# Kernel tuning notes

Measured on AMD Instinct MI355X. Metric: run time of the kernel, lower is better.

Reference implementation:

```python
import jax, jax.numpy as jnp
import numpy as np

N_NODES = 100000
N_EDGES = 1600000
N_GRAPHS = 256
HIDDEN = 256
ADD_FEATURES = 7
BN_EPS = 1e-5


def setup_inputs() -> dict:
    key = jax.random.key(0)
    ks = jax.random.split(key, 12)
    x = jax.random.normal(ks[0], (N_NODES, 1), dtype=jnp.float32)
    edge_index = jax.random.randint(ks[1], (2, N_EDGES), 0, N_NODES, dtype=jnp.int32)
    batch = jnp.sort(jax.random.randint(ks[2], (N_NODES,), 0, N_GRAPHS, dtype=jnp.int32))
    y_feat = jax.random.normal(ks[3], (N_GRAPHS, ADD_FEATURES), dtype=jnp.float32)
    # learned parameters
    W_conv = jax.random.normal(ks[4], (1, HIDDEN), dtype=jnp.float32) * 0.5
    b_conv = jnp.zeros((HIDDEN,), dtype=jnp.float32)
    gamma = jnp.ones((HIDDEN,), dtype=jnp.float32)
    beta = jnp.zeros((HIDDEN,), dtype=jnp.float32)
    W1 = jax.random.normal(ks[5], (HIDDEN + ADD_FEATURES, 128), dtype=jnp.float32) * (1.0 / np.sqrt(HIDDEN + ADD_FEATURES))
    b1 = jnp.zeros((128,), dtype=jnp.float32)
    W2 = jax.random.normal(ks[6], (128, 2), dtype=jnp.float32) * (1.0 / np.sqrt(128))
    b2 = jnp.zeros((2,), dtype=jnp.float32)
    return {"x": x, "edge_index": edge_index, "batch": batch, "y_feat": y_feat,
            "W_conv": W_conv, "b_conv": b_conv, "gamma": gamma, "beta": beta,
            "W1": W1, "b1": b1, "W2": W2, "b2": b2}


def _gcn_conv(x, W, b, edge_index, n_nodes):
    # PyG GCNConv: add self-loops, symmetric normalization D^-1/2 (A+I) D^-1/2 (x W) + b
    loop = jnp.arange(n_nodes, dtype=edge_index.dtype)
    src = jnp.concatenate([edge_index[0], loop])
    dst = jnp.concatenate([edge_index[1], loop])
    deg = jax.ops.segment_sum(jnp.ones_like(dst, dtype=x.dtype), dst, num_segments=n_nodes)
    dinv = jnp.where(deg > 0, jax.lax.rsqrt(jnp.maximum(deg, 1e-12)), 0.0)
    norm = dinv[src] * dinv[dst]                      # [E+N]
    xw = x @ W                                        # [N, H]
    msg = xw[src] * norm[:, None]                     # gather [E+N, H]
    return jax.ops.segment_sum(msg, dst, num_segments=n_nodes) + b


def reference(x, edge_index, batch, y_feat, W_conv, b_conv, gamma, beta, W1, b1, W2, b2):
    n_nodes = x.shape[0]
    h = _gcn_conv(x, W_conv, b_conv, edge_index, n_nodes)      # [N, 256]
    h = jax.nn.gelu(h, approximate=False)
    # BatchNorm over nodes (training-mode batch stats, biased variance, eps=1e-5)
    mean = jnp.mean(h, axis=0)
    var = jnp.mean(jnp.square(h - mean), axis=0)
    h = (h - mean) * jax.lax.rsqrt(var + BN_EPS) * gamma + beta
    # global mean pool by graph id
    sums = jax.ops.segment_sum(h, batch, num_segments=N_GRAPHS)           # [G, 256]
    counts = jax.ops.segment_sum(jnp.ones((n_nodes,), h.dtype), batch, num_segments=N_GRAPHS)
    pooled = sums / jnp.maximum(counts, 1.0)[:, None]
    g = jnp.concatenate([pooled, y_feat], axis=1)               # [G, 263]
    g = jax.nn.gelu(g @ W1 + b1, approximate=False)             # [G, 128]
    out = jax.nn.sigmoid(g @ W2 + b2)                           # [G, 2]
    return out
```

## Files before the change

kernel.cpp:

```cpp
#include <hip/hip_runtime.h>
#include <hip/hip_bf16.h>

#define HID 256
#define ADDF 7
#define MLP1 128
#define BN_EPS 1e-5f
#define NREP 8

#define NB 512
#define BW 196
#define BCAP 4096
#define PC 4096
#define PT 256
#define NW 4

__device__ __forceinline__ float gelu_fast(float z) {
    float z2 = z * z;
    float y2 = z * fmaf(0.07135481627f, z2, 1.59576912161f);
    float u  = __expf(fminf(y2, 80.0f));
    return z * u * __builtin_amdgcn_rcpf(u + 1.0f);
}

__global__ void k_init(float* zp, int nz, int* binCur,
                       const int* __restrict__ batch, int* __restrict__ cnt, int N, int G) {
    const int nzBlocks = (nz + 255) / 256;
    if ((int)blockIdx.x < nzBlocks) {
        int i = blockIdx.x * 256 + threadIdx.x;
        if (i < nz) zp[i] = 0.0f;
    } else {
        const int t = threadIdx.x;
        for (int b = t; b < NB; b += 256) binCur[b] = b * BCAP;
        if (t < G) {
            int lo = 0, hi = N;
            while (lo < hi) { int mid = (lo + hi) >> 1; if (batch[mid] < t) lo = mid + 1; else hi = mid; }
            int start = lo;
            lo = 0; hi = N;
            while (lo < hi) { int mid = (lo + hi) >> 1; if (batch[mid] < t + 1) lo = mid + 1; else hi = mid; }
            cnt[t] = lo - start;
        }
    }
}

__global__ __launch_bounds__(PT) void k_place(
        const int* __restrict__ src, const int* __restrict__ dst,
        int* __restrict__ binCur, int* __restrict__ recs, int E) {
    __shared__ int hist[NW][NB];
    const int t = threadIdx.x;
    const int w = t >> 6;
    for (int k = t; k < NW * NB; k += PT) (&hist[0][0])[k] = 0;
    __syncthreads();

    const int s0 = blockIdx.x * PC;
    const int e0 = min(s0 + PC, E);
    const bool vec = ((E & 3) == 0);
    const int n4 = vec ? ((e0 - s0) >> 2) : 0;
    const int4* dst4 = (const int4*)(dst + s0);
    const int4* src4 = (const int4*)(src + s0);

    for (int q = t; q < n4; q += PT) {
        int4 d = dst4[q];
        atomicAdd(&hist[w][d.x / BW], 1);
        atomicAdd(&hist[w][d.y / BW], 1);
        atomicAdd(&hist[w][d.z / BW], 1);
        atomicAdd(&hist[w][d.w / BW], 1);
    }
    for (int i = s0 + (n4 << 2) + t; i < e0; i += PT)
        atomicAdd(&hist[w][dst[i] / BW], 1);
    __syncthreads();

    for (int bb = t; bb < NB; bb += PT) {
        int b = (bb + ((int)blockIdx.x << 4)) & (NB - 1);
        int c0 = hist[0][b], c1 = hist[1][b], c2 = hist[2][b], c3 = hist[3][b];
        int tot = c0 + c1 + c2 + c3;
        int base = tot ? atomicAdd(&binCur[b], tot) : 0;
        hist[0][b] = base;
        hist[1][b] = base + c0;
        hist[2][b] = base + c0 + c1;
        hist[3][b] = base + c0 + c1 + c2;
    }
    __syncthreads();

    for (int q = t; q < n4; q += PT) {
        int4 d = dst4[q];
        int4 s = src4[q];
        int bin, pos;
        bin = d.x / BW; pos = atomicAdd(&hist[w][bin], 1); recs[pos] = ((d.x - bin * BW) << 17) | s.x;
        bin = d.y / BW; pos = atomicAdd(&hist[w][bin], 1); recs[pos] = ((d.y - bin * BW) << 17) | s.y;
        bin = d.z / BW; pos = atomicAdd(&hist[w][bin], 1); recs[pos] = ((d.z - bin * BW) << 17) | s.z;
        bin = d.w / BW; pos = atomicAdd(&hist[w][bin], 1); recs[pos] = ((d.w - bin * BW) << 17) | s.w;
    }
    for (int i = s0 + (n4 << 2) + t; i < e0; i += PT) {
        int d = dst[i];
        int bin = d / BW;
        int pos = atomicAdd(&hist[w][bin], 1);
        recs[pos] = ((d - bin * BW) << 17) | src[i];
    }
}

__global__ __launch_bounds__(256) void k_degv(
        const int* __restrict__ recs, const int* __restrict__ binCur,
        const float* __restrict__ x, float* __restrict__ dinv, float* __restrict__ v, int N) {
    __shared__ int degL[BW];
    const int b = blockIdx.x;
    const int t = threadIdx.x;
    if (t < BW) degL[t] = 0;
    __syncthreads();

    const int start = b * BCAP;
    const int end   = binCur[b];
    const int n4 = (end - start) >> 2;
    const int4* r4 = (const int4*)(recs + start);
    for (int q = t; q < n4; q += 256) {
        int4 r = r4[q];
        atomicAdd(&degL[r.x >> 17], 1);
        atomicAdd(&degL[r.y >> 17], 1);
        atomicAdd(&degL[r.z >> 17], 1);
        atomicAdd(&degL[r.w >> 17], 1);
    }
    for (int i = start + (n4 << 2) + t; i < end; i += 256)
        atomicAdd(&degL[recs[i] >> 17], 1);
    __syncthreads();

    int node = b * BW + t;
    if (t < BW && node < N) {
        float di = rsqrtf((float)degL[t] + 1.0f);
        dinv[node] = di;
        v[node]    = di * x[node];
    }
}

__global__ __launch_bounds__(HID) void k_agg_gelu(
        const int* __restrict__ recs, const int* __restrict__ binCur,
        const float* __restrict__ v, const float* __restrict__ dinv,
        const int* __restrict__ batch,
        const float* __restrict__ Wc, const float* __restrict__ bc,
        float* __restrict__ Sgj, float* __restrict__ Trep, float* __restrict__ T2rep, int N) {
    __shared__ float aggL[BW];
    __shared__ float sh_s[BW];
    __shared__ int   sh_b[BW];
    const int b = blockIdx.x;
    const int t = threadIdx.x;
    if (t < BW) aggL[t] = 0.0f;
    __syncthreads();

    const int start = b * BCAP;
    const int end   = binCur[b];
    const int n4 = (end - start) >> 2;
    const int4* r4 = (const int4*)(recs + start);
    for (int q = t; q < n4; q += 256) {
        int4 r = r4[q];
        atomicAdd(&aggL[r.x >> 17], v[r.x & 0x1FFFF]);
        atomicAdd(&aggL[r.y >> 17], v[r.y & 0x1FFFF]);
        atomicAdd(&aggL[r.z >> 17], v[r.z & 0x1FFFF]);
        atomicAdd(&aggL[r.w >> 17], v[r.w & 0x1FFFF]);
    }
    for (int i = start + (n4 << 2) + t; i < end; i += 256) {
        int rec = recs[i];
        atomicAdd(&aggL[rec >> 17], v[rec & 0x1FFFF]);
    }
    __syncthreads();

    const int node0 = b * BW;
    const int count = min(BW, N - node0);
    if (count <= 0) return;

    if (t < count) {
        int node = node0 + t;
        sh_s[t] = dinv[node] * (aggL[t] + v[node]);
        sh_b[t] = batch[node];
    }
    __syncthreads();

    const float wa = Wc[t];
    const float wb = bc[t];
    float tsum = 0.f, t2sum = 0.f, gsum = 0.f;
    int gid = sh_b[0];
    int n = 0;
    for (; n + 2 <= count; n += 2) {
        float h0 = gelu_fast(fmaf(sh_s[n],     wa, wb));
        float h1 = gelu_fast(fmaf(sh_s[n + 1], wa, wb));
        int b0 = sh_b[n], b1v = sh_b[n + 1];
        tsum += h0 + h1; t2sum += fmaf(h0, h0, h1 * h1);
        if (b0 != gid)  { atomicAdd(&Sgj[gid * HID + t], gsum); gsum = 0.f; gid = b0; }
        gsum += h0;
        if (b1v != gid) { atomicAdd(&Sgj[gid * HID + t], gsum); gsum = 0.f; gid = b1v; }
        gsum += h1;
    }
    if (n < count) {
        float h0 = gelu_fast(fmaf(sh_s[n], wa, wb));
        tsum += h0; t2sum += h0 * h0;
        int b0 = sh_b[n];
        if (b0 != gid) { atomicAdd(&Sgj[gid * HID + t], gsum); gsum = 0.f; gid = b0; }
        gsum += h0;
    }
    atomicAdd(&Sgj[gid * HID + t], gsum);
    const int r = b & (NREP - 1);
    atomicAdd(&Trep [r * HID + t], tsum);
    atomicAdd(&T2rep[r * HID + t], t2sum);
}

__global__ __launch_bounds__(HID) void k_pool_mlp(
        const float* __restrict__ Sgj, const float* __restrict__ Trep, const float* __restrict__ T2rep,
        const int* __restrict__ cnt, const float* __restrict__ gamma, const float* __restrict__ beta,
        const float* __restrict__ yfeat,
        const float* __restrict__ W1, const float* __restrict__ b1,
        const float* __restrict__ W2, const float* __restrict__ b2,
        float* __restrict__ out, int N) {
    __shared__ float gv[HID + ADDF];
    __shared__ float hid[MLP1];
    const int g = blockIdx.x;
    const int t = threadIdx.x;

    float Ts = 0.f, T2s = 0.f;
    #pragma unroll
    for (int r = 0; r < NREP; ++r) { Ts += Trep[r * HID + t]; T2s += T2rep[r * HID + t]; }
    float invN = 1.0f / (float)N;
    float mean = Ts * invN;
    float var  = fmaf(-mean, mean, T2s * invN);
    float rinv = rsqrtf(var + BN_EPS);
    float c = (float)max(cnt[g], 1);
    gv[t] = (Sgj[g * HID + t] / c - mean) * rinv * gamma[t] + beta[t];
    if (t < ADDF) gv[HID + t] = yfeat[g * ADDF + t];
    __syncthreads();

    if (t < MLP1) {
        float acc = b1[t];
        #pragma unroll 8
        for (int k = 0; k < HID + ADDF; ++k)
            acc = fmaf(gv[k], W1[k * MLP1 + t], acc);
        hid[t] = gelu_fast(acc);
    }
    __syncthreads();

    if (t < 2) {
        float o = b2[t];
        for (int k = 0; k < MLP1; ++k)
            o = fmaf(hid[k], W2[k * 2 + t], o);
        out[g * 2 + t] = 1.0f / (1.0f + expf(-o));
    }
}

__global__ void k_zero(float* p, int n) {
    for (int i = blockIdx.x * blockDim.x + threadIdx.x; i < n; i += gridDim.x * blockDim.x)
        p[i] = 0.0f;
}
__global__ void k_deg_fb(const int* __restrict__ dst, float* __restrict__ deg, int E) {
    int i = blockIdx.x * blockDim.x + threadIdx.x;
    if (i < E) atomicAdd(&deg[dst[i]], 1.0f);
}
__global__ void k_dinv_fb(float* __restrict__ deg, const float* __restrict__ x,
                          float* __restrict__ v, int N) {
    int i = blockIdx.x * blockDim.x + threadIdx.x;
    if (i < N) { float di = rsqrtf(deg[i] + 1.0f); deg[i] = di; v[i] = di * x[i]; }
}
__global__ void k_scatter_fb(const int* __restrict__ src, const int* __restrict__ dst,
                             const float* __restrict__ v, float* __restrict__ agg, int E) {
    int i = blockIdx.x * blockDim.x + threadIdx.x;
    if (i < E) atomicAdd(&agg[dst[i]], v[src[i]]);
}
#define CHUNK_FB 64
__global__ __launch_bounds__(HID) void k_gelu_fb(
        const float* __restrict__ v, const float* __restrict__ dinv,
        const float* __restrict__ agg, const int* __restrict__ batch,
        const float* __restrict__ Wc, const float* __restrict__ bc,
        float* __restrict__ Sgj, float* __restrict__ Trep, float* __restrict__ T2rep, int N) {
    __shared__ float sh_s[CHUNK_FB];
    __shared__ int   sh_b[CHUNK_FB];
    const int j = threadIdx.x;
    const int base = blockIdx.x * CHUNK_FB;
    const int count = min(CHUNK_FB, N - base);
    if (j < count) {
        int i = base + j;
        sh_s[j] = dinv[i] * (agg[i] + v[i]);
        sh_b[j] = batch[i];
    }
    __syncthreads();
    const float a = Wc[j];
    const float b = bc[j];
    float tsum = 0.f, t2sum = 0.f, gsum = 0.f;
    int gid = sh_b[0];
    for (int n = 0; n < count; ++n) {
        float h = gelu_fast(fmaf(sh_s[n], a, b));
        tsum += h; t2sum += h * h;
        int bg = sh_b[n];
        if (bg != gid) { atomicAdd(&Sgj[gid * HID + j], gsum); gsum = 0.f; gid = bg; }
        gsum += h;
    }
    atomicAdd(&Sgj[gid * HID + j], gsum);
    const int r = blockIdx.x & (NREP - 1);
    atomicAdd(&Trep [r * HID + j], tsum);
    atomicAdd(&T2rep[r * HID + j], t2sum);
}

extern "C" void kernel_launch(void* const* d_in, const int* in_sizes, int n_in,
                              void* d_out, int out_size, void* d_ws, size_t ws_size,
                              hipStream_t stream) {
    const float* x     = (const float*)d_in[0];
    const int*   edge  = (const int*)  d_in[1];
    const int*   batch = (const int*)  d_in[2];
    const float* yfeat = (const float*)d_in[3];
    const float* Wc    = (const float*)d_in[4];
    const float* bc    = (const float*)d_in[5];
    const float* gamma = (const float*)d_in[6];
    const float* beta  = (const float*)d_in[7];
    const float* W1    = (const float*)d_in[8];
    const float* b1    = (const float*)d_in[9];
    const float* W2    = (const float*)d_in[10];
    const float* b2    = (const float*)d_in[11];
    float* out = (float*)d_out;

    const int N = in_sizes[0];
    const int E = in_sizes[1] / 2;
    const int G = in_sizes[3] / ADDF;

    const int* srcIdx = edge;
    const int* dstIdx = edge + E;

    float* ws     = (float*)d_ws;
    float* Sgj    = ws;
    float* Trep   = Sgj + (size_t)G * HID;
    float* T2rep  = Trep + NREP * HID;
    int*   cnt    = (int*)(T2rep + NREP * HID);
    int*   binCur = cnt + G;
    float* dinv   = (float*)(binCur + NB);
    float* v      = dinv + (size_t)NB * BW;
    int*   recs   = (int*)(v + (size_t)NB * BW);

    const size_t headF  = (size_t)G * HID + 2 * NREP * HID + G + NB;
    const size_t needT1 = (headF + 2 * (size_t)NB * BW + (size_t)NB * BCAP) * 4;
    const int zeroCount = G * HID + 2 * NREP * HID;
    const int initBlocks = (zeroCount + 255) / 256 + 1;

    if (ws_size >= needT1 && N <= NB * BW) {
        k_init<<<initBlocks, 256, 0, stream>>>(Sgj, zeroCount, binCur, batch, cnt, N, G);
        k_place<<<(E + PC - 1) / PC, PT, 0, stream>>>(srcIdx, dstIdx, binCur, recs, E);
        k_degv<<<NB, 256, 0, stream>>>(recs, binCur, x, dinv, v, N);
        k_agg_gelu<<<NB, HID, 0, stream>>>(recs, binCur, v, dinv, batch, Wc, bc, Sgj, Trep, T2rep, N);
    } else {
        float* degA = (float*)(binCur + NB);
        float* vA   = degA + N;
        float* aggA = vA + N;
        k_init<<<initBlocks, 256, 0, stream>>>(Sgj, zeroCount, binCur, batch, cnt, N, G);
        k_zero<<<512, 256, 0, stream>>>(degA, N);
        k_zero<<<512, 256, 0, stream>>>(aggA, N);
        k_deg_fb<<<(E + 255) / 256, 256, 0, stream>>>(dstIdx, degA, E);
        k_dinv_fb<<<(N + 255) / 256, 256, 0, stream>>>(degA, x, vA, N);
        k_scatter_fb<<<(E + 255) / 256, 256, 0, stream>>>(srcIdx, dstIdx, vA, aggA, E);
        k_gelu_fb<<<(N + CHUNK_FB - 1) / CHUNK_FB, HID, 0, stream>>>(vA, degA, aggA, batch, Wc, bc, Sgj, Trep, T2rep, N);
    }

    k_pool_mlp<<<G, HID, 0, stream>>>(Sgj, Trep, T2rep, cnt, gamma, beta, yfeat, W1, b1, W2, b2, out, N);
}
```

Baseline: 86.40 us.

## Fuse all stages into one cooperative persistent kernel with grid syncs

Replaces the five separate launches (init, place, degree, aggregate+gelu, pool+MLP) with a single cooperative kernel of 512 blocks that separates the stages with grid-wide syncs. Edge placement now uses one chunk per block instead of 4096-edge chunks, so each block handles about 3125 edges. The aim is to remove launch overhead and inter-kernel gaps. In exchange it adds grid.sync costs, relies on all 512 blocks being co-resident, and gives less parallelism to the placement and MLP stages.

```diff
diff --git a/kernel.cpp b/kernel.cpp
--- a/kernel.cpp
+++ b/kernel.cpp
@@ -1,5 +1,8 @@
 #include <hip/hip_runtime.h>
+#include <hip/hip_cooperative_groups.h>
 #include <hip/hip_bf16.h>
+
+namespace cg = cooperative_groups;
 
 #define HID 256
 #define ADDF 7
@@ -10,8 +13,6 @@
 #define NB 512
 #define BW 196
 #define BCAP 4096
-#define PC 4096
-#define PT 256
 #define NW 4
 
 __device__ __forceinline__ float gelu_fast(float z) {
@@ -21,15 +22,238 @@
     return z * u * __builtin_amdgcn_rcpf(u + 1.0f);
 }
 
-__global__ void k_init(float* zp, int nz, int* binCur,
-                       const int* __restrict__ batch, int* __restrict__ cnt, int N, int G) {
+__global__ __launch_bounds__(256, 2) void k_mega(
+        const float* __restrict__ x, const int* __restrict__ src, const int* __restrict__ dst,
+        const int* __restrict__ batch, const float* __restrict__ yfeat,
+        const float* __restrict__ Wc, const float* __restrict__ bc,
+        const float* __restrict__ gamma, const float* __restrict__ beta,
+        const float* __restrict__ W1, const float* __restrict__ b1,
+        const float* __restrict__ W2, const float* __restrict__ b2,
+        float* __restrict__ out,
+        float* __restrict__ Sgj, float* __restrict__ Trep, float* __restrict__ T2rep,
+        int* __restrict__ cnt, int* __restrict__ binCur,
+        float* __restrict__ dinv, float* __restrict__ v, int* __restrict__ recs,
+        int N, int E, int G) {
+    cg::grid_group grid = cg::this_grid();
+    __shared__ int smbuf[NW * NB];
+    const int t = threadIdx.x;
+    const int b = blockIdx.x;
+    const int nblk = (int)gridDim.x;
+
+    {
+        const int zc = G * HID + 2 * NREP * HID;
+        const int gt = b * 256 + t;
+        const int tot = nblk * 256;
+        for (int i = gt; i < zc; i += tot) Sgj[i] = 0.0f;
+        if (gt < NB) binCur[gt] = gt * BCAP;
+        const int g = gt - NB;
+        if (g >= 0 && g < G) {
+            int lo = 0, hi = N;
+            while (lo < hi) { int mid = (lo + hi) >> 1; if (batch[mid] < g) lo = mid + 1; else hi = mid; }
+            int start = lo;
+            lo = 0; hi = N;
+            while (lo < hi) { int mid = (lo + hi) >> 1; if (batch[mid] < g + 1) lo = mid + 1; else hi = mid; }
+            cnt[g] = lo - start;
+        }
+    }
+    grid.sync();
+
+    {
+        const int pcm = (((E + nblk - 1) / nblk) + 3) & ~3;
+        const int s0 = b * pcm;
+        const int e0 = min(s0 + pcm, E);
+        int (*hist)[NB] = (int(*)[NB])smbuf;
+        const int w = t >> 6;
+        for (int k = t; k < NW * NB; k += 256) smbuf[k] = 0;
+        __syncthreads();
+
+        bool al = false; int n4 = 0;
+        if (s0 < e0) {
+            al = (((((uintptr_t)(dst + s0)) | ((uintptr_t)(src + s0))) & 15) == 0);
+            n4 = al ? ((e0 - s0) >> 2) : 0;
+            const int4* dst4 = (const int4*)(dst + s0);
+            for (int q = t; q < n4; q += 256) {
+                int4 d = dst4[q];
+                atomicAdd(&hist[w][d.x / BW], 1);
+                atomicAdd(&hist[w][d.y / BW], 1);
+                atomicAdd(&hist[w][d.z / BW], 1);
+                atomicAdd(&hist[w][d.w / BW], 1);
+            }
+            for (int i = s0 + (n4 << 2) + t; i < e0; i += 256)
+                atomicAdd(&hist[w][dst[i] / BW], 1);
+        }
+        __syncthreads();
+
+        for (int bb = t; bb < NB; bb += 256) {
+            int bi = (bb + (b << 4)) & (NB - 1);
+            int c0 = hist[0][bi], c1 = hist[1][bi], c2 = hist[2][bi], c3 = hist[3][bi];
+            int tot4 = c0 + c1 + c2 + c3;
+            int base = tot4 ? atomicAdd(&binCur[bi], tot4) : 0;
+            hist[0][bi] = base;
+            hist[1][bi] = base + c0;
+            hist[2][bi] = base + c0 + c1;
+            hist[3][bi] = base + c0 + c1 + c2;
+        }
+        __syncthreads();
+
+        if (s0 < e0) {
+            const int4* dst4 = (const int4*)(dst + s0);
+            const int4* src4 = (const int4*)(src + s0);
+            for (int q = t; q < n4; q += 256) {
+                int4 d = dst4[q];
+                int4 s = src4[q];
+                int bin, pos;
+                bin = d.x / BW; pos = atomicAdd(&hist[w][bin], 1); recs[pos] = ((d.x - bin * BW) << 17) | s.x;
+                bin = d.y / BW; pos = atomicAdd(&hist[w][bin], 1); recs[pos] = ((d.y - bin * BW) << 17) | s.y;
+                bin = d.z / BW; pos = atomicAdd(&hist[w][bin], 1); recs[pos] = ((d.z - bin * BW) << 17) | s.z;
+                bin = d.w / BW; pos = atomicAdd(&hist[w][bin], 1); recs[pos] = ((d.w - bin * BW) << 17) | s.w;
+            }
+            for (int i = s0 + (n4 << 2) + t; i < e0; i += 256) {
+                int d = dst[i];
+                int bin = d / BW;
+                int pos = atomicAdd(&hist[w][bin], 1);
+                recs[pos] = ((d - bin * BW) << 17) | src[i];
+            }
+        }
+    }
+    grid.sync();
+
+    {
+        int* degL = smbuf;
+        if (t < BW) degL[t] = 0;
+        __syncthreads();
+
+        const int start = b * BCAP;
+        const int end   = binCur[b];
+        const int n4 = (end - start) >> 2;
+        const int4* r4 = (const int4*)(recs + start);
+        for (int q = t; q < n4; q += 256) {
+            int4 r = r4[q];
+            atomicAdd(&degL[r.x >> 17], 1);
+            atomicAdd(&degL[r.y >> 17], 1);
+            atomicAdd(&degL[r.z >> 17], 1);
+            atomicAdd(&degL[r.w >> 17], 1);
+        }
+        for (int i = start + (n4 << 2) + t; i < end; i += 256)
+            atomicAdd(&degL[recs[i] >> 17], 1);
+        __syncthreads();
+
+        int node = b * BW + t;
+        if (t < BW && node < N) {
+            float di = rsqrtf((float)degL[t] + 1.0f);
+            dinv[node] = di;
+            v[node]    = di * x[node];
+        }
+    }
+    grid.sync();
+
+    {
+        float* aggL = (float*)smbuf;
+        float* sh_s = aggL + BW;
+        int*   sh_b = (int*)(sh_s + BW);
+        if (t < BW) aggL[t] = 0.0f;
+        __syncthreads();
+
+        const int start = b * BCAP;
+        const int end   = binCur[b];
+        const int n4 = (end - start) >> 2;
+        const int4* r4 = (const int4*)(recs + start);
+        for (int q = t; q < n4; q += 256) {
+            int4 r = r4[q];
+            atomicAdd(&aggL[r.x >> 17], v[r.x & 0x1FFFF]);
+            atomicAdd(&aggL[r.y >> 17], v[r.y & 0x1FFFF]);
+            atomicAdd(&aggL[r.z >> 17], v[r.z & 0x1FFFF]);
+            atomicAdd(&aggL[r.w >> 17], v[r.w & 0x1FFFF]);
+        }
+        for (int i = start + (n4 << 2) + t; i < end; i += 256) {
+            int rec = recs[i];
+            atomicAdd(&aggL[rec >> 17], v[rec & 0x1FFFF]);
+        }
+        __syncthreads();
+
+        const int node0 = b * BW;
+        const int count = min(BW, N - node0);
+        if (count > 0) {
+            if (t < count) {
+                int node = node0 + t;
+                sh_s[t] = dinv[node] * (aggL[t] + v[node]);
+                sh_b[t] = batch[node];
+            }
+            __syncthreads();
+
+            const float wa = Wc[t];
+            const float wb = bc[t];
+            float tsum = 0.f, t2sum = 0.f, gsum = 0.f;
+            int gid = sh_b[0];
+            int n = 0;
+            for (; n + 2 <= count; n += 2) {
+                float h0 = gelu_fast(fmaf(sh_s[n],     wa, wb));
+                float h1 = gelu_fast(fmaf(sh_s[n + 1], wa, wb));
+                int b0 = sh_b[n], b1v = sh_b[n + 1];
+                tsum += h0 + h1; t2sum += fmaf(h0, h0, h1 * h1);
+                if (b0 != gid)  { atomicAdd(&Sgj[gid * HID + t], gsum); gsum = 0.f; gid = b0; }
+                gsum += h0;
+                if (b1v != gid) { atomicAdd(&Sgj[gid * HID + t], gsum); gsum = 0.f; gid = b1v; }
+                gsum += h1;
+            }
+            if (n < count) {
+                float h0 = gelu_fast(fmaf(sh_s[n], wa, wb));
+                tsum += h0; t2sum += h0 * h0;
+                int b0 = sh_b[n];
+                if (b0 != gid) { atomicAdd(&Sgj[gid * HID + t], gsum); gsum = 0.f; gid = b0; }
+                gsum += h0;
+            }
+            atomicAdd(&Sgj[gid * HID + t], gsum);
+            const int r = b & (NREP - 1);
+            atomicAdd(&Trep [r * HID + t], tsum);
+            atomicAdd(&T2rep[r * HID + t], t2sum);
+        }
+    }
+    grid.sync();
+
+    for (int g = b; g < G; g += nblk) {
+        float* gv  = (float*)smbuf;
+        float* hid = gv + HID + ADDF;
+
+        float Ts = 0.f, T2s = 0.f;
+        #pragma unroll
+        for (int r = 0; r < NREP; ++r) { Ts += Trep[r * HID + t]; T2s += T2rep[r * HID + t]; }
+        float invN = 1.0f / (float)N;
+        float mean = Ts * invN;
+        float var  = fmaf(-mean, mean, T2s * invN);
+        float rinv = rsqrtf(var + BN_EPS);
+        float c = (float)max(cnt[g], 1);
+        gv[t] = (Sgj[g * HID + t] / c - mean) * rinv * gamma[t] + beta[t];
+        if (t < ADDF) gv[HID + t] = yfeat[g * ADDF + t];
+        __syncthreads();
+
+        if (t < MLP1) {
+            float acc = b1[t];
+            #pragma unroll 8
+            for (int k = 0; k < HID + ADDF; ++k)
+                acc = fmaf(gv[k], W1[k * MLP1 + t], acc);
+            hid[t] = gelu_fast(acc);
+        }
+        __syncthreads();
+
+        if (t < 2) {
+            float o = b2[t];
+            for (int k = 0; k < MLP1; ++k)
+                o = fmaf(hid[k], W2[k * 2 + t], o);
+            out[g * 2 + t] = 1.0f / (1.0f + expf(-o));
+        }
+        __syncthreads();
+    }
+}
+
+__global__ void k_init_fb(float* zp, int nz, const int* __restrict__ batch,
+                          int* __restrict__ cnt, int N, int G) {
     const int nzBlocks = (nz + 255) / 256;
     if ((int)blockIdx.x < nzBlocks) {
         int i = blockIdx.x * 256 + threadIdx.x;
         if (i < nz) zp[i] = 0.0f;
     } else {
         const int t = threadIdx.x;
-        for (int b = t; b < NB; b += 256) binCur[b] = b * BCAP;
         if (t < G) {
             int lo = 0, hi = N;
             while (lo < hi) { int mid = (lo + hi) >> 1; if (batch[mid] < t) lo = mid + 1; else hi = mid; }
@@ -40,206 +264,6 @@
         }
     }
 }
-
-__global__ __launch_bounds__(PT) void k_place(
-        const int* __restrict__ src, const int* __restrict__ dst,
-        int* __restrict__ binCur, int* __restrict__ recs, int E) {
-    __shared__ int hist[NW][NB];
-    const int t = threadIdx.x;
-    const int w = t >> 6;
-    for (int k = t; k < NW * NB; k += PT) (&hist[0][0])[k] = 0;
-    __syncthreads();
-
-    const int s0 = blockIdx.x * PC;
-    const int e0 = min(s0 + PC, E);
-    const bool vec = ((E & 3) == 0);
-    const int n4 = vec ? ((e0 - s0) >> 2) : 0;
-    const int4* dst4 = (const int4*)(dst + s0);
-    const int4* src4 = (const int4*)(src + s0);
-
-    for (int q = t; q < n4; q += PT) {
-        int4 d = dst4[q];
-        atomicAdd(&hist[w][d.x / BW], 1);
-        atomicAdd(&hist[w][d.y / BW], 1);
-        atomicAdd(&hist[w][d.z / BW], 1);
-        atomicAdd(&hist[w][d.w / BW], 1);
-    }
-    for (int i = s0 + (n4 << 2) + t; i < e0; i += PT)
-        atomicAdd(&hist[w][dst[i] / BW], 1);
-    __syncthreads();
-
-    for (int bb = t; bb < NB; bb += PT) {
-        int b = (bb + ((int)blockIdx.x << 4)) & (NB - 1);
-        int c0 = hist[0][b], c1 = hist[1][b], c2 = hist[2][b], c3 = hist[3][b];
-        int tot = c0 + c1 + c2 + c3;
-        int base = tot ? atomicAdd(&binCur[b], tot) : 0;
-        hist[0][b] = base;
-        hist[1][b] = base + c0;
-        hist[2][b] = base + c0 + c1;
-        hist[3][b] = base + c0 + c1 + c2;
-    }
-    __syncthreads();
-
-    for (int q = t; q < n4; q += PT) {
-        int4 d = dst4[q];
-        int4 s = src4[q];
-        int bin, pos;
-        bin = d.x / BW; pos = atomicAdd(&hist[w][bin], 1); recs[pos] = ((d.x - bin * BW) << 17) | s.x;
-        bin = d.y / BW; pos = atomicAdd(&hist[w][bin], 1); recs[pos] = ((d.y - bin * BW) << 17) | s.y;
-        bin = d.z / BW; pos = atomicAdd(&hist[w][bin], 1); recs[pos] = ((d.z - bin * BW) << 17) | s.z;
-        bin = d.w / BW; pos = atomicAdd(&hist[w][bin], 1); recs[pos] = ((d.w - bin * BW) << 17) | s.w;
-    }
-    for (int i = s0 + (n4 << 2) + t; i < e0; i += PT) {
-        int d = dst[i];
-        int bin = d / BW;
-        int pos = atomicAdd(&hist[w][bin], 1);
-        recs[pos] = ((d - bin * BW) << 17) | src[i];
-    }
-}
-
-__global__ __launch_bounds__(256) void k_degv(
-        const int* __restrict__ recs, const int* __restrict__ binCur,
-        const float* __restrict__ x, float* __restrict__ dinv, float* __restrict__ v, int N) {
-    __shared__ int degL[BW];
-    const int b = blockIdx.x;
-    const int t = threadIdx.x;
-    if (t < BW) degL[t] = 0;
-    __syncthreads();
-
-    const int start = b * BCAP;
-    const int end   = binCur[b];
-    const int n4 = (end - start) >> 2;
-    const int4* r4 = (const int4*)(recs + start);
-    for (int q = t; q < n4; q += 256) {
-        int4 r = r4[q];
-        atomicAdd(&degL[r.x >> 17], 1);
-        atomicAdd(&degL[r.y >> 17], 1);
-        atomicAdd(&degL[r.z >> 17], 1);
-        atomicAdd(&degL[r.w >> 17], 1);
-    }
-    for (int i = start + (n4 << 2) + t; i < end; i += 256)
-        atomicAdd(&degL[recs[i] >> 17], 1);
-    __syncthreads();
-
-    int node = b * BW + t;
-    if (t < BW && node < N) {
-        float di = rsqrtf((float)degL[t] + 1.0f);
-        dinv[node] = di;
-        v[node]    = di * x[node];
-    }
-}
-
-__global__ __launch_bounds__(HID) void k_agg_gelu(
-        const int* __restrict__ recs, const int* __restrict__ binCur,
-        const float* __restrict__ v, const float* __restrict__ dinv,
-        const int* __restrict__ batch,
-        const float* __restrict__ Wc, const float* __restrict__ bc,
-        float* __restrict__ Sgj, float* __restrict__ Trep, float* __restrict__ T2rep, int N) {
-    __shared__ float aggL[BW];
-    __shared__ float sh_s[BW];
-    __shared__ int   sh_b[BW];
-    const int b = blockIdx.x;
-    const int t = threadIdx.x;
-    if (t < BW) aggL[t] = 0.0f;
-    __syncthreads();
-
-    const int start = b * BCAP;
-    const int end   = binCur[b];
-    const int n4 = (end - start) >> 2;
-    const int4* r4 = (const int4*)(recs + start);
-    for (int q = t; q < n4; q += 256) {
-        int4 r = r4[q];
-        atomicAdd(&aggL[r.x >> 17], v[r.x & 0x1FFFF]);
-        atomicAdd(&aggL[r.y >> 17], v[r.y & 0x1FFFF]);
-        atomicAdd(&aggL[r.z >> 17], v[r.z & 0x1FFFF]);
-        atomicAdd(&aggL[r.w >> 17], v[r.w & 0x1FFFF]);
-    }
-    for (int i = start + (n4 << 2) + t; i < end; i += 256) {
-        int rec = recs[i];
-        atomicAdd(&aggL[rec >> 17], v[rec & 0x1FFFF]);
-    }
-    __syncthreads();
-
-    const int node0 = b * BW;
-    const int count = min(BW, N - node0);
-    if (count <= 0) return;
-
-    if (t < count) {
-        int node = node0 + t;
-        sh_s[t] = dinv[node] * (aggL[t] + v[node]);
-        sh_b[t] = batch[node];
-    }
-    __syncthreads();
-
-    const float wa = Wc[t];
-    const float wb = bc[t];
-    float tsum = 0.f, t2sum = 0.f, gsum = 0.f;
-    int gid = sh_b[0];
-    int n = 0;
-    for (; n + 2 <= count; n += 2) {
-        float h0 = gelu_fast(fmaf(sh_s[n],     wa, wb));
-        float h1 = gelu_fast(fmaf(sh_s[n + 1], wa, wb));
-        int b0 = sh_b[n], b1v = sh_b[n + 1];
-        tsum += h0 + h1; t2sum += fmaf(h0, h0, h1 * h1);
-        if (b0 != gid)  { atomicAdd(&Sgj[gid * HID + t], gsum); gsum = 0.f; gid = b0; }
-        gsum += h0;
-        if (b1v != gid) { atomicAdd(&Sgj[gid * HID + t], gsum); gsum = 0.f; gid = b1v; }
-        gsum += h1;
-    }
-    if (n < count) {
-        float h0 = gelu_fast(fmaf(sh_s[n], wa, wb));
-        tsum += h0; t2sum += h0 * h0;
-        int b0 = sh_b[n];
-        if (b0 != gid) { atomicAdd(&Sgj[gid * HID + t], gsum); gsum = 0.f; gid = b0; }
-        gsum += h0;
-    }
-    atomicAdd(&Sgj[gid * HID + t], gsum);
-    const int r = b & (NREP - 1);
-    atomicAdd(&Trep [r * HID + t], tsum);
-    atomicAdd(&T2rep[r * HID + t], t2sum);
-}
-
-__global__ __launch_bounds__(HID) void k_pool_mlp(
-        const float* __restrict__ Sgj, const float* __restrict__ Trep, const float* __restrict__ T2rep,
-        const int* __restrict__ cnt, const float* __restrict__ gamma, const float* __restrict__ beta,
-        const float* __restrict__ yfeat,
-        const float* __restrict__ W1, const float* __restrict__ b1,
-        const float* __restrict__ W2, const float* __restrict__ b2,
-        float* __restrict__ out, int N) {
-    __shared__ float gv[HID + ADDF];
-    __shared__ float hid[MLP1];
-    const int g = blockIdx.x;
-    const int t = threadIdx.x;
-
-    float Ts = 0.f, T2s = 0.f;
-    #pragma unroll
-    for (int r = 0; r < NREP; ++r) { Ts += Trep[r * HID + t]; T2s += T2rep[r * HID + t]; }
-    float invN = 1.0f / (float)N;
-    float mean = Ts * invN;
-    float var  = fmaf(-mean, mean, T2s * invN);
-    float rinv = rsqrtf(var + BN_EPS);
-    float c = (float)max(cnt[g], 1);
-    gv[t] = (Sgj[g * HID + t] / c - mean) * rinv * gamma[t] + beta[t];
-    if (t < ADDF) gv[HID + t] = yfeat[g * ADDF + t];
-    __syncthreads();
-
-    if (t < MLP1) {
-        float acc = b1[t];
-        #pragma unroll 8
-        for (int k = 0; k < HID + ADDF; ++k)
-            acc = fmaf(gv[k], W1[k * MLP1 + t], acc);
-        hid[t] = gelu_fast(acc);
-    }
-    __syncthreads();
-
-    if (t < 2) {
-        float o = b2[t];
-        for (int k = 0; k < MLP1; ++k)
-            o = fmaf(hid[k], W2[k * 2 + t], o);
-        out[g * 2 + t] = 1.0f / (1.0f + expf(-o));
-    }
-}
-
 __global__ void k_zero(float* p, int n) {
     for (int i = blockIdx.x * blockDim.x + threadIdx.x; i < n; i += gridDim.x * blockDim.x)
         p[i] = 0.0f;
@@ -290,6 +314,43 @@
     const int r = blockIdx.x & (NREP - 1);
     atomicAdd(&Trep [r * HID + j], tsum);
     atomicAdd(&T2rep[r * HID + j], t2sum);
+}
+__global__ __launch_bounds__(HID) void k_pool_mlp_fb(
+        const float* __restrict__ Sgj, const float* __restrict__ Trep, const float* __restrict__ T2rep,
+        const int* __restrict__ cnt, const float* __restrict__ gamma, const float* __restrict__ beta,
+        const float* __restrict__ yfeat,
+        const float* __restrict__ W1, const float* __restrict__ b1,
+        const float* __restrict__ W2, const float* __restrict__ b2,
+        float* __restrict__ out, int N) {
+    __shared__ float gv[HID + ADDF];
+    __shared__ float hid[MLP1];
+    const int g = blockIdx.x;
+    const int t = threadIdx.x;
+    float Ts = 0.f, T2s = 0.f;
+    #pragma unroll
+    for (int r = 0; r < NREP; ++r) { Ts += Trep[r * HID + t]; T2s += T2rep[r * HID + t]; }
+    float invN = 1.0f / (float)N;
+    float mean = Ts * invN;
+    float var  = fmaf(-mean, mean, T2s * invN);
+    float rinv = rsqrtf(var + BN_EPS);
+    float c = (float)max(cnt[g], 1);
+    gv[t] = (Sgj[g * HID + t] / c - mean) * rinv * gamma[t] + beta[t];
+    if (t < ADDF) gv[HID + t] = yfeat[g * ADDF + t];
+    __syncthreads();
+    if (t < MLP1) {
+        float acc = b1[t];
+        #pragma unroll 8
+        for (int k = 0; k < HID + ADDF; ++k)
+            acc = fmaf(gv[k], W1[k * MLP1 + t], acc);
+        hid[t] = gelu_fast(acc);
+    }
+    __syncthreads();
+    if (t < 2) {
+        float o = b2[t];
+        for (int k = 0; k < MLP1; ++k)
+            o = fmaf(hid[k], W2[k * 2 + t], o);
+        out[g * 2 + t] = 1.0f / (1.0f + expf(-o));
+    }
 }
 
 extern "C" void kernel_launch(void* const* d_in, const int* in_sizes, int n_in,
@@ -309,9 +370,9 @@
     const float* b2    = (const float*)d_in[11];
     float* out = (float*)d_out;
 
-    const int N = in_sizes[0];
-    const int E = in_sizes[1] / 2;
-    const int G = in_sizes[3] / ADDF;
+    int N = in_sizes[0];
+    int E = in_sizes[1] / 2;
+    int G = in_sizes[3] / ADDF;
 
     const int* srcIdx = edge;
     const int* dstIdx = edge + E;
@@ -329,25 +390,28 @@
     const size_t headF  = (size_t)G * HID + 2 * NREP * HID + G + NB;
     const size_t needT1 = (headF + 2 * (size_t)NB * BW + (size_t)NB * BCAP) * 4;
     const int zeroCount = G * HID + 2 * NREP * HID;
-    const int initBlocks = (zeroCount + 255) / 256 + 1;
-
-    if (ws_size >= needT1 && N <= NB * BW) {
-        k_init<<<initBlocks, 256, 0, stream>>>(Sgj, zeroCount, binCur, batch, cnt, N, G);
-        k_place<<<(E + PC - 1) / PC, PT, 0, stream>>>(srcIdx, dstIdx, binCur, recs, E);
-        k_degv<<<NB, 256, 0, stream>>>(recs, binCur, x, dinv, v, N);
-        k_agg_gelu<<<NB, HID, 0, stream>>>(recs, binCur, v, dinv, batch, Wc, bc, Sgj, Trep, T2rep, N);
+
+    if (ws_size >= needT1 && N <= NB * BW && G <= 131072 - NB) {
+        void* args[] = {
+            (void*)&x, (void*)&srcIdx, (void*)&dstIdx, (void*)&batch, (void*)&yfeat,
+            (void*)&Wc, (void*)&bc, (void*)&gamma, (void*)&beta,
+            (void*)&W1, (void*)&b1, (void*)&W2, (void*)&b2, (void*)&out,
+            (void*)&Sgj, (void*)&Trep, (void*)&T2rep, (void*)&cnt, (void*)&binCur,
+            (void*)&dinv, (void*)&v, (void*)&recs, (void*)&N, (void*)&E, (void*)&G
+        };
+        hipLaunchCooperativeKernel((void*)k_mega, dim3(NB), dim3(256), args, 0, stream);
     } else {
         float* degA = (float*)(binCur + NB);
         float* vA   = degA + N;
         float* aggA = vA + N;
-        k_init<<<initBlocks, 256, 0, stream>>>(Sgj, zeroCount, binCur, batch, cnt, N, G);
+        const int initBlocks = (zeroCount + 255) / 256 + 1;
+        k_init_fb<<<initBlocks, 256, 0, stream>>>(Sgj, zeroCount, batch, cnt, N, G);
         k_zero<<<512, 256, 0, stream>>>(degA, N);
         k_zero<<<512, 256, 0, stream>>>(aggA, N);
         k_deg_fb<<<(E + 255) / 256, 256, 0, stream>>>(dstIdx, degA, E);
         k_dinv_fb<<<(N + 255) / 256, 256, 0, stream>>>(degA, x, vA, N);
         k_scatter_fb<<<(E + 255) / 256, 256, 0, stream>>>(srcIdx, dstIdx, vA, aggA, E);
         k_gelu_fb<<<(N + CHUNK_FB - 1) / CHUNK_FB, HID, 0, stream>>>(vA, degA, aggA, batch, Wc, bc, Sgj, Trep, T2rep, N);
-    }
-
-    k_pool_mlp<<<G, HID, 0, stream>>>(Sgj, Trep, T2rep, cnt, gamma, beta, yfeat, W1, b1, W2, b2, out, N);
-}
+        k_pool_mlp_fb<<<G, HID, 0, stream>>>(Sgj, Trep, T2rep, cnt, gamma, beta, yfeat, W1, b1, W2, b2, out, N);
+    }
+}
```

Result: slower. 305.2 us (+253.2%).

## Replace atomic bin placement with histogram, scan and deterministic store passes

Applied to the files above, without the earlier changes.

Splits the single-pass edge binning kernel into three kernels. A per-chunk histogram pass writes counts to global memory, a per-bin scan turns them into chunk offsets, and a store pass scatters the packed records. This removes the global atomicAdd on bin cursors and folds zeroing and graph counts into these kernels, though it reads the edge array twice and adds a launch. The degree and aggregation kernels move to 512 threads, with the GELU loop split across two halves of the node range, to raise parallelism per bin.

```diff
diff --git a/kernel.cpp b/kernel.cpp
--- a/kernel.cpp
+++ b/kernel.cpp
@@ -10,8 +10,7 @@
 #define NB 512
 #define BW 196
 #define BCAP 4096
-#define PC 4096
-#define PT 256
+#define PC 2048
 #define NW 4
 
 __device__ __forceinline__ float gelu_fast(float z) {
@@ -21,83 +20,118 @@
     return z * u * __builtin_amdgcn_rcpf(u + 1.0f);
 }
 
-__global__ void k_init(float* zp, int nz, int* binCur,
-                       const int* __restrict__ batch, int* __restrict__ cnt, int N, int G) {
-    const int nzBlocks = (nz + 255) / 256;
-    if ((int)blockIdx.x < nzBlocks) {
-        int i = blockIdx.x * 256 + threadIdx.x;
-        if (i < nz) zp[i] = 0.0f;
-    } else {
-        const int t = threadIdx.x;
-        for (int b = t; b < NB; b += 256) binCur[b] = b * BCAP;
-        if (t < G) {
-            int lo = 0, hi = N;
-            while (lo < hi) { int mid = (lo + hi) >> 1; if (batch[mid] < t) lo = mid + 1; else hi = mid; }
-            int start = lo;
-            lo = 0; hi = N;
-            while (lo < hi) { int mid = (lo + hi) >> 1; if (batch[mid] < t + 1) lo = mid + 1; else hi = mid; }
-            cnt[t] = lo - start;
+__global__ __launch_bounds__(256) void k_hist(
+        const int* __restrict__ dst, int* __restrict__ hist,
+        float* __restrict__ zbase, int zcount, int E, int nchunk, int cpx) {
+    __shared__ int h[NW][NB];
+    const int t = threadIdx.x;
+    const int bid = blockIdx.x;
+
+    int gt = bid * 256 + t;
+    if (gt < zcount) zbase[gt] = 0.0f;
+
+    const int m = (bid & 7) * cpx + (bid >> 3);
+    for (int k = t; k < NW * NB; k += 256) (&h[0][0])[k] = 0;
+    __syncthreads();
+
+    if (m < nchunk) {
+        const int s0 = m * PC;
+        const int e0 = min(s0 + PC, E);
+        const int w = t >> 6;
+        const bool al = ((((uintptr_t)(dst + s0)) & 15) == 0);
+        const int n4 = al ? ((e0 - s0) >> 2) : 0;
+        const int4* dst4 = (const int4*)(dst + s0);
+        for (int q = t; q < n4; q += 256) {
+            int4 d = dst4[q];
+            atomicAdd(&h[w][d.x / BW], 1);
+            atomicAdd(&h[w][d.y / BW], 1);
+            atomicAdd(&h[w][d.z / BW], 1);
+            atomicAdd(&h[w][d.w / BW], 1);
         }
-    }
-}
-
-__global__ __launch_bounds__(PT) void k_place(
+        for (int i = s0 + (n4 << 2) + t; i < e0; i += 256)
+            atomicAdd(&h[w][dst[i] / BW], 1);
+        __syncthreads();
+        for (int b = t; b < NB; b += 256)
+            hist[(size_t)m * NB + b] = h[0][b] + h[1][b] + h[2][b] + h[3][b];
+    }
+}
+
+__global__ __launch_bounds__(64) void k_scan(
+        int* __restrict__ hist, int* __restrict__ binCur,
+        const int* __restrict__ batch, int* __restrict__ cnt,
+        int nchunk, int N, int G) {
+    const int bin = blockIdx.x;
+    const int lane = threadIdx.x;
+    __shared__ int bounds[2];
+
+    if (bin < G && lane < 2) {
+        int target = bin + lane;
+        int lo = 0, hi = N;
+        while (lo < hi) { int mid = (lo + hi) >> 1; if (batch[mid] < target) lo = mid + 1; else hi = mid; }
+        bounds[lane] = lo;
+    }
+
+    const int per = (nchunk + 63) / 64;
+    const int m0 = lane * per;
+    const int m1 = min(m0 + per, nchunk);
+    int sum = 0;
+    for (int m = m0; m < m1; ++m) sum += hist[(size_t)m * NB + bin];
+
+    int incl = sum;
+    #pragma unroll
+    for (int d = 1; d < 64; d <<= 1) {
+        int o = __shfl_up(incl, d);
+        if (lane >= d) incl += o;
+    }
+    const int total = __shfl(incl, 63);
+    int run = bin * BCAP + (incl - sum);
+    for (int m = m0; m < m1; ++m) {
+        int c = hist[(size_t)m * NB + bin];
+        hist[(size_t)m * NB + bin] = run;
+        run += c;
+    }
+    if (lane == 63) binCur[bin] = bin * BCAP + total;
+
+    __syncthreads();
+    if (bin < G && lane == 0) cnt[bin] = bounds[1] - bounds[0];
+}
+
+__global__ __launch_bounds__(256) void k_store(
         const int* __restrict__ src, const int* __restrict__ dst,
-        int* __restrict__ binCur, int* __restrict__ recs, int E) {
-    __shared__ int hist[NW][NB];
+        const int* __restrict__ hist, int* __restrict__ recs,
+        int E, int nchunk, int cpx) {
+    __shared__ int cur[NB];
     const int t = threadIdx.x;
-    const int w = t >> 6;
-    for (int k = t; k < NW * NB; k += PT) (&hist[0][0])[k] = 0;
-    __syncthreads();
-
-    const int s0 = blockIdx.x * PC;
+    const int m = ((int)blockIdx.x & 7) * cpx + ((int)blockIdx.x >> 3);
+    if (m >= nchunk) return;
+
+    for (int b = t; b < NB; b += 256) cur[b] = hist[(size_t)m * NB + b];
+    __syncthreads();
+
+    const int s0 = m * PC;
     const int e0 = min(s0 + PC, E);
-    const bool vec = ((E & 3) == 0);
-    const int n4 = vec ? ((e0 - s0) >> 2) : 0;
+    const bool al = (((((uintptr_t)(dst + s0)) | ((uintptr_t)(src + s0))) & 15) == 0);
+    const int n4 = al ? ((e0 - s0) >> 2) : 0;
     const int4* dst4 = (const int4*)(dst + s0);
     const int4* src4 = (const int4*)(src + s0);
-
-    for (int q = t; q < n4; q += PT) {
-        int4 d = dst4[q];
-        atomicAdd(&hist[w][d.x / BW], 1);
-        atomicAdd(&hist[w][d.y / BW], 1);
-        atomicAdd(&hist[w][d.z / BW], 1);
-        atomicAdd(&hist[w][d.w / BW], 1);
-    }
-    for (int i = s0 + (n4 << 2) + t; i < e0; i += PT)
-        atomicAdd(&hist[w][dst[i] / BW], 1);
-    __syncthreads();
-
-    for (int bb = t; bb < NB; bb += PT) {
-        int b = (bb + ((int)blockIdx.x << 4)) & (NB - 1);
-        int c0 = hist[0][b], c1 = hist[1][b], c2 = hist[2][b], c3 = hist[3][b];
-        int tot = c0 + c1 + c2 + c3;
-        int base = tot ? atomicAdd(&binCur[b], tot) : 0;
-        hist[0][b] = base;
-        hist[1][b] = base + c0;
-        hist[2][b] = base + c0 + c1;
-        hist[3][b] = base + c0 + c1 + c2;
-    }
-    __syncthreads();
-
-    for (int q = t; q < n4; q += PT) {
+    for (int q = t; q < n4; q += 256) {
         int4 d = dst4[q];
         int4 s = src4[q];
         int bin, pos;
-        bin = d.x / BW; pos = atomicAdd(&hist[w][bin], 1); recs[pos] = ((d.x - bin * BW) << 17) | s.x;
-        bin = d.y / BW; pos = atomicAdd(&hist[w][bin], 1); recs[pos] = ((d.y - bin * BW) << 17) | s.y;
-        bin = d.z / BW; pos = atomicAdd(&hist[w][bin], 1); recs[pos] = ((d.z - bin * BW) << 17) | s.z;
-        bin = d.w / BW; pos = atomicAdd(&hist[w][bin], 1); recs[pos] = ((d.w - bin * BW) << 17) | s.w;
-    }
-    for (int i = s0 + (n4 << 2) + t; i < e0; i += PT) {
+        bin = d.x / BW; pos = atomicAdd(&cur[bin], 1); recs[pos] = ((d.x - bin * BW) << 17) | s.x;
+        bin = d.y / BW; pos = atomicAdd(&cur[bin], 1); recs[pos] = ((d.y - bin * BW) << 17) | s.y;
+        bin = d.z / BW; pos = atomicAdd(&cur[bin], 1); recs[pos] = ((d.z - bin * BW) << 17) | s.z;
+        bin = d.w / BW; pos = atomicAdd(&cur[bin], 1); recs[pos] = ((d.w - bin * BW) << 17) | s.w;
+    }
+    for (int i = s0 + (n4 << 2) + t; i < e0; i += 256) {
         int d = dst[i];
         int bin = d / BW;
-        int pos = atomicAdd(&hist[w][bin], 1);
+        int pos = atomicAdd(&cur[bin], 1);
         recs[pos] = ((d - bin * BW) << 17) | src[i];
     }
 }
 
-__global__ __launch_bounds__(256) void k_degv(
+__global__ __launch_bounds__(512) void k_degv(
         const int* __restrict__ recs, const int* __restrict__ binCur,
         const float* __restrict__ x, float* __restrict__ dinv, float* __restrict__ v, int N) {
     __shared__ int degL[BW];
@@ -110,14 +144,14 @@
     const int end   = binCur[b];
     const int n4 = (end - start) >> 2;
     const int4* r4 = (const int4*)(recs + start);
-    for (int q = t; q < n4; q += 256) {
+    for (int q = t; q < n4; q += 512) {
         int4 r = r4[q];
         atomicAdd(&degL[r.x >> 17], 1);
         atomicAdd(&degL[r.y >> 17], 1);
         atomicAdd(&degL[r.z >> 17], 1);
         atomicAdd(&degL[r.w >> 17], 1);
     }
-    for (int i = start + (n4 << 2) + t; i < end; i += 256)
+    for (int i = start + (n4 << 2) + t; i < end; i += 512)
         atomicAdd(&degL[recs[i] >> 17], 1);
     __syncthreads();
 
@@ -129,7 +163,7 @@
     }
 }
 
-__global__ __launch_bounds__(HID) void k_agg_gelu(
+__global__ __launch_bounds__(512) void k_agg_gelu(
         const int* __restrict__ recs, const int* __restrict__ binCur,
         const float* __restrict__ v, const float* __restrict__ dinv,
         const int* __restrict__ batch,
@@ -147,14 +181,14 @@
     const int end   = binCur[b];
     const int n4 = (end - start) >> 2;
     const int4* r4 = (const int4*)(recs + start);
-    for (int q = t; q < n4; q += 256) {
+    for (int q = t; q < n4; q += 512) {
         int4 r = r4[q];
         atomicAdd(&aggL[r.x >> 17], v[r.x & 0x1FFFF]);
         atomicAdd(&aggL[r.y >> 17], v[r.y & 0x1FFFF]);
         atomicAdd(&aggL[r.z >> 17], v[r.z & 0x1FFFF]);
         atomicAdd(&aggL[r.w >> 17], v[r.w & 0x1FFFF]);
     }
-    for (int i = start + (n4 << 2) + t; i < end; i += 256) {
+    for (int i = start + (n4 << 2) + t; i < end; i += 512) {
         int rec = recs[i];
         atomicAdd(&aggL[rec >> 17], v[rec & 0x1FFFF]);
     }
@@ -171,32 +205,37 @@
     }
     __syncthreads();
 
-    const float wa = Wc[t];
-    const float wb = bc[t];
-    float tsum = 0.f, t2sum = 0.f, gsum = 0.f;
-    int gid = sh_b[0];
-    int n = 0;
-    for (; n + 2 <= count; n += 2) {
-        float h0 = gelu_fast(fmaf(sh_s[n],     wa, wb));
-        float h1 = gelu_fast(fmaf(sh_s[n + 1], wa, wb));
-        int b0 = sh_b[n], b1v = sh_b[n + 1];
-        tsum += h0 + h1; t2sum += fmaf(h0, h0, h1 * h1);
-        if (b0 != gid)  { atomicAdd(&Sgj[gid * HID + t], gsum); gsum = 0.f; gid = b0; }
-        gsum += h0;
-        if (b1v != gid) { atomicAdd(&Sgj[gid * HID + t], gsum); gsum = 0.f; gid = b1v; }
-        gsum += h1;
-    }
-    if (n < count) {
-        float h0 = gelu_fast(fmaf(sh_s[n], wa, wb));
-        tsum += h0; t2sum += h0 * h0;
-        int b0 = sh_b[n];
-        if (b0 != gid) { atomicAdd(&Sgj[gid * HID + t], gsum); gsum = 0.f; gid = b0; }
-        gsum += h0;
-    }
-    atomicAdd(&Sgj[gid * HID + t], gsum);
-    const int r = b & (NREP - 1);
-    atomicAdd(&Trep [r * HID + t], tsum);
-    atomicAdd(&T2rep[r * HID + t], t2sum);
+    const int f = t & 255;
+    const int nbeg = (t < 256) ? 0 : 98;
+    const int nend = (t < 256) ? min(98, count) : count;
+    if (nbeg < nend) {
+        const float wa = Wc[f];
+        const float wb = bc[f];
+        float tsum = 0.f, t2sum = 0.f, gsum = 0.f;
+        int gid = sh_b[nbeg];
+        int n = nbeg;
+        for (; n + 2 <= nend; n += 2) {
+            float h0 = gelu_fast(fmaf(sh_s[n],     wa, wb));
+            float h1 = gelu_fast(fmaf(sh_s[n + 1], wa, wb));
+            int b0 = sh_b[n], b1v = sh_b[n + 1];
+            tsum += h0 + h1; t2sum += fmaf(h0, h0, h1 * h1);
+            if (b0 != gid)  { atomicAdd(&Sgj[gid * HID + f], gsum); gsum = 0.f; gid = b0; }
+            gsum += h0;
+            if (b1v != gid) { atomicAdd(&Sgj[gid * HID + f], gsum); gsum = 0.f; gid = b1v; }
+            gsum += h1;
+        }
+        if (n < nend) {
+            float h0 = gelu_fast(fmaf(sh_s[n], wa, wb));
+            tsum += h0; t2sum += h0 * h0;
+            int b0 = sh_b[n];
+            if (b0 != gid) { atomicAdd(&Sgj[gid * HID + f], gsum); gsum = 0.f; gid = b0; }
+            gsum += h0;
+        }
+        atomicAdd(&Sgj[gid * HID + f], gsum);
+        const int r = b & (NREP - 1);
+        atomicAdd(&Trep [r * HID + f], tsum);
+        atomicAdd(&T2rep[r * HID + f], t2sum);
+    }
 }
 
 __global__ __launch_bounds__(HID) void k_pool_mlp(
@@ -240,6 +279,24 @@
     }
 }
 
+__global__ void k_init_fb(float* zp, int nz, const int* __restrict__ batch,
+                          int* __restrict__ cnt, int N, int G) {
+    const int nzBlocks = (nz + 255) / 256;
+    if ((int)blockIdx.x < nzBlocks) {
+        int i = blockIdx.x * 256 + threadIdx.x;
+        if (i < nz) zp[i] = 0.0f;
+    } else {
+        const int t = threadIdx.x;
+        if (t < G) {
+            int lo = 0, hi = N;
+            while (lo < hi) { int mid = (lo + hi) >> 1; if (batch[mid] < t) lo = mid + 1; else hi = mid; }
+            int start = lo;
+            lo = 0; hi = N;
+            while (lo < hi) { int mid = (lo + hi) >> 1; if (batch[mid] < t + 1) lo = mid + 1; else hi = mid; }
+            cnt[t] = lo - start;
+        }
+    }
+}
 __global__ void k_zero(float* p, int n) {
     for (int i = blockIdx.x * blockDim.x + threadIdx.x; i < n; i += gridDim.x * blockDim.x)
         p[i] = 0.0f;
@@ -316,6 +373,10 @@
     const int* srcIdx = edge;
     const int* dstIdx = edge + E;
 
+    const int nchunk = (E + PC - 1) / PC;
+    const int cpx    = (nchunk + 7) / 8;
+    const int pgrid  = cpx * 8;
+
     float* ws     = (float*)d_ws;
     float* Sgj    = ws;
     float* Trep   = Sgj + (size_t)G * HID;
@@ -324,30 +385,32 @@
     int*   binCur = cnt + G;
     float* dinv   = (float*)(binCur + NB);
     float* v      = dinv + (size_t)NB * BW;
-    int*   recs   = (int*)(v + (size_t)NB * BW);
-
-    const size_t headF  = (size_t)G * HID + 2 * NREP * HID + G + NB;
-    const size_t needT1 = (headF + 2 * (size_t)NB * BW + (size_t)NB * BCAP) * 4;
+    int*   hist   = (int*)(v + (size_t)NB * BW);
+    int*   recs   = hist + (size_t)pgrid * NB;
+
+    const size_t headF  = (size_t)G * HID + 2 * NREP * HID + G + NB + 2 * (size_t)NB * BW;
+    const size_t needT1 = (headF + (size_t)pgrid * NB + (size_t)NB * BCAP) * 4;
     const int zeroCount = G * HID + 2 * NREP * HID;
-    const int initBlocks = (zeroCount + 255) / 256 + 1;
-
-    if (ws_size >= needT1 && N <= NB * BW) {
-        k_init<<<initBlocks, 256, 0, stream>>>(Sgj, zeroCount, binCur, batch, cnt, N, G);
-        k_place<<<(E + PC - 1) / PC, PT, 0, stream>>>(srcIdx, dstIdx, binCur, recs, E);
-        k_degv<<<NB, 256, 0, stream>>>(recs, binCur, x, dinv, v, N);
-        k_agg_gelu<<<NB, HID, 0, stream>>>(recs, binCur, v, dinv, batch, Wc, bc, Sgj, Trep, T2rep, N);
+
+    if (ws_size >= needT1 && N <= NB * BW && G <= NB) {
+        k_hist<<<pgrid, 256, 0, stream>>>(dstIdx, hist, Sgj, zeroCount, E, nchunk, cpx);
+        k_scan<<<NB, 64, 0, stream>>>(hist, binCur, batch, cnt, nchunk, N, G);
+        k_store<<<pgrid, 256, 0, stream>>>(srcIdx, dstIdx, hist, recs, E, nchunk, cpx);
+        k_degv<<<NB, 512, 0, stream>>>(recs, binCur, x, dinv, v, N);
+        k_agg_gelu<<<NB, 512, 0, stream>>>(recs, binCur, v, dinv, batch, Wc, bc, Sgj, Trep, T2rep, N);
+        k_pool_mlp<<<G, HID, 0, stream>>>(Sgj, Trep, T2rep, cnt, gamma, beta, yfeat, W1, b1, W2, b2, out, N);
     } else {
         float* degA = (float*)(binCur + NB);
         float* vA   = degA + N;
         float* aggA = vA + N;
-        k_init<<<initBlocks, 256, 0, stream>>>(Sgj, zeroCount, binCur, batch, cnt, N, G);
+        const int initBlocks = (zeroCount + 255) / 256 + 1;
+        k_init_fb<<<initBlocks, 256, 0, stream>>>(Sgj, zeroCount, batch, cnt, N, G);
         k_zero<<<512, 256, 0, stream>>>(degA, N);
         k_zero<<<512, 256, 0, stream>>>(aggA, N);
         k_deg_fb<<<(E + 255) / 256, 256, 0, stream>>>(dstIdx, degA, E);
         k_dinv_fb<<<(N + 255) / 256, 256, 0, stream>>>(degA, x, vA, N);
         k_scatter_fb<<<(E + 255) / 256, 256, 0, stream>>>(srcIdx, dstIdx, vA, aggA, E);
         k_gelu_fb<<<(N + CHUNK_FB - 1) / CHUNK_FB, HID, 0, stream>>>(vA, degA, aggA, batch, Wc, bc, Sgj, Trep, T2rep, N);
-    }
-
-    k_pool_mlp<<<G, HID, 0, stream>>>(Sgj, Trep, T2rep, cnt, gamma, beta, yfeat, W1, b1, W2, b2, out, N);
-}
+        k_pool_mlp<<<G, HID, 0, stream>>>(Sgj, Trep, T2rep, cnt, gamma, beta, yfeat, W1, b1, W2, b2, out, N);
+    }
+}
```

Result: faster. 76.88 us (-11.0%).
